# Performance work log

Hardware: AMD Instinct MI355X
Metric: run time of the kernel (lower is better)

Reference implementation:

```python
import jax, jax.numpy as jnp
import numpy as np

N = 50000        # num nodes
E = 800000       # num edges (before self-loops)
IN = 256         # in_channels
HID = 32         # hidden_channels per head
HEADS = 8
OUT = 64         # out_channels (layer 2, heads=1)
NEG_SLOPE = 0.2  # PyG GATConv default leaky_relu slope


def setup_inputs() -> dict:
    key = jax.random.key(0)
    ks = jax.random.split(key, 12)
    def rn(k, shape, scale=0.1):
        return jax.random.normal(k, shape, dtype=jnp.float32) * scale
    x = jax.random.normal(ks[0], (N, IN), dtype=jnp.float32)
    edge_index = jax.random.randint(ks[1], (2, E), 0, N, dtype=jnp.int64)
    return {
        "x": x,
        "edge_index": edge_index,
        # GATConv 1: in=256 -> 32 per head, 8 heads, concat
        "W1": rn(ks[2], (IN, HEADS * HID)),
        "att_src1": rn(ks[3], (HEADS, HID)),
        "att_dst1": rn(ks[4], (HEADS, HID)),
        "b1": jnp.zeros((HEADS * HID,), jnp.float32),
        # GATConv 2: in=256 -> 64, 1 head
        "W2": rn(ks[5], (HEADS * HID, OUT)),
        "att_src2": rn(ks[6], (1, OUT)),
        "att_dst2": rn(ks[7], (1, OUT)),
        "b2": jnp.zeros((OUT,), jnp.float32),
    }


def _gat_conv(x, src, dst, W, att_src, att_dst, bias, heads, out_ch):
    """PyG-style GATConv (add_self_loops already applied to src/dst).
    x: [N, F_in]; src/dst: [E']; returns [N, heads*out_ch] (concat)."""
    n = x.shape[0]
    h = (x @ W).reshape(n, heads, out_ch)                     # [N,H,F]
    a_src = jnp.einsum('nhf,hf->nh', h, att_src)              # [N,H]
    a_dst = jnp.einsum('nhf,hf->nh', h, att_dst)
    e = jax.nn.leaky_relu(a_src[src] + a_dst[dst], NEG_SLOPE)  # [E',H]
    # scatter-softmax over incoming edges of each dst node
    m = jax.ops.segment_max(e, dst, num_segments=n)            # [N,H]
    ex = jnp.exp(e - m[dst])
    denom = jax.ops.segment_sum(ex, dst, num_segments=n)       # [N,H]
    alpha = ex / denom[dst]                                    # [E',H]
    msg = alpha[:, :, None] * h[src]                           # [E',H,F]
    out = jax.ops.segment_sum(msg, dst, num_segments=n)        # [N,H,F]
    return out.reshape(n, heads * out_ch) + bias


def reference(x, edge_index, W1, att_src1, att_dst1, b1, W2, att_src2, att_dst2, b2):
    n = x.shape[0]
    loop = jnp.arange(n, dtype=edge_index.dtype)
    src = jnp.concatenate([edge_index[0], loop])  # add self-loops (PyG default)
    dst = jnp.concatenate([edge_index[1], loop])
    h = _gat_conv(x, src, dst, W1, att_src1, att_dst1, b1, HEADS, HID)
    h = jax.nn.relu(h)
    out = _gat_conv(h, src, dst, W2, att_src2, att_dst2, b2, 1, OUT)
    return out
```

## Files before the change

### kernel.cpp

```cpp
#include <hip/hip_runtime.h>
#include <hip/hip_bf16.h>


#define HEADS 8
#define HID 32
#define F1 256
#define F2 64
#define NEG_SLOPE 0.2f
#define SCAN_CHUNK 1024

typedef __attribute__((ext_vector_type(8))) short bf16x8;
typedef __attribute__((ext_vector_type(4))) float f32x4;
typedef __attribute__((ext_vector_type(8))) unsigned short u16x8;

__device__ __forceinline__ unsigned short f2b(float f) {
    union { float f; unsigned int i; } x; x.f = f;
    unsigned int r = x.i + 0x7fffu + ((x.i >> 16) & 1u);
    return (unsigned short)(r >> 16);
}
__device__ __forceinline__ float b2f(unsigned short u) {
    union { unsigned int i; float f; } x; x.i = ((unsigned int)u) << 16;
    return x.f;
}
__device__ __forceinline__ float leaky(float v) {
    return v > 0.f ? v : NEG_SLOPE * v;
}

__global__ void setup_kernel(const float* __restrict__ W1,
                             const float* __restrict__ W2,
                             unsigned short* __restrict__ W1T,
                             unsigned short* __restrict__ W2T,
                             int* __restrict__ deg, int Nn) {
    const int i = blockIdx.x * 256 + threadIdx.x;
    if (i < F1 * F1) {
        const int k = i >> 8, n = i & (F1 - 1);
        W1T[(size_t)n * F1 + k] = f2b(W1[i]);
    } else if (i < F1 * F1 + F1 * F2) {
        const int j = i - F1 * F1;
        const int k = j >> 6, n = j & (F2 - 1);
        W2T[(size_t)n * F1 + k] = f2b(W2[j]);
    } else if (i < F1 * F1 + F1 * F2 + Nn) {
        deg[i - F1 * F1 - F1 * F2] = 0;
    }
}

template<int BN, bool A_FP32, bool OUT_BF16>
__global__ __launch_bounds__(256) void mfma_gemm(
        const void* __restrict__ A,
        const unsigned short* __restrict__ BT,
        void* __restrict__ C, int M, int N, int K) {
    constexpr int BM = 128, BK = 32;
    __shared__ unsigned short As[BM * BK];
    __shared__ unsigned short Bs[BN * BK];
    const int tid = threadIdx.x;
    const int wave = tid >> 6, lane = tid & 63;
    const int quad = lane >> 4, l16 = lane & 15;
    const int brow = blockIdx.x * BM;
    const int bcol = blockIdx.y * BN;

    constexpr int MI = (BN == 128) ? 4 : 2;
    constexpr int NJ = 4;
    const int wm = (BN == 128) ? (wave & 1) * 64 : wave * 32;
    const int wn = (BN == 128) ? (wave >> 1) * 64 : 0;

    f32x4 acc[MI][NJ] = {};

    for (int k0 = 0; k0 < K; k0 += BK) {
#pragma unroll
        for (int it = 0; it < (BM * BK) / (256 * 8); ++it) {
            const int idx = it * 256 + tid;
            const int r = idx >> 2;
            const int kk = (idx & 3) * 8;
            const int gr = brow + r;
            if (A_FP32) {
                const float* Af = (const float*)A;
                float4 a0 = make_float4(0.f, 0.f, 0.f, 0.f);
                float4 a1 = make_float4(0.f, 0.f, 0.f, 0.f);
                if (gr < M) {
                    a0 = *(const float4*)&Af[(size_t)gr * K + k0 + kk];
                    a1 = *(const float4*)&Af[(size_t)gr * K + k0 + kk + 4];
                }
                ushort4 lo, hi;
                lo.x = f2b(a0.x); lo.y = f2b(a0.y); lo.z = f2b(a0.z); lo.w = f2b(a0.w);
                hi.x = f2b(a1.x); hi.y = f2b(a1.y); hi.z = f2b(a1.z); hi.w = f2b(a1.w);
                *(ushort4*)&As[r * BK + kk] = lo;
                *(ushort4*)&As[r * BK + kk + 4] = hi;
            } else {
                const unsigned short* Ab = (const unsigned short*)A;
                uint4 v = make_uint4(0u, 0u, 0u, 0u);
                if (gr < M) v = *(const uint4*)&Ab[(size_t)gr * K + k0 + kk];
                *(uint4*)&As[r * BK + kk] = v;
            }
        }
#pragma unroll
        for (int it = 0; it < (BN * BK) / (256 * 8); ++it) {
            const int idx = it * 256 + tid;
            const int r = idx >> 2;
            const int kk = (idx & 3) * 8;
            const uint4 v = *(const uint4*)&BT[(size_t)(bcol + r) * K + k0 + kk];
            *(uint4*)&Bs[r * BK + kk] = v;
        }
        __syncthreads();
        bf16x8 af[MI], bfr[NJ];
#pragma unroll
        for (int i = 0; i < MI; ++i)
            af[i] = *(const bf16x8*)&As[(wm + i * 16 + l16) * BK + quad * 8];
#pragma unroll
        for (int j = 0; j < NJ; ++j)
            bfr[j] = *(const bf16x8*)&Bs[(wn + j * 16 + l16) * BK + quad * 8];
#pragma unroll
        for (int i = 0; i < MI; ++i)
#pragma unroll
            for (int j = 0; j < NJ; ++j)
                acc[i][j] = __builtin_amdgcn_mfma_f32_16x16x32_bf16(
                    af[i], bfr[j], acc[i][j], 0, 0, 0);
        __syncthreads();
    }
#pragma unroll
    for (int i = 0; i < MI; ++i) {
#pragma unroll
        for (int r = 0; r < 4; ++r) {
            const int row = brow + wm + i * 16 + quad * 4 + r;
            if (row >= M) continue;
#pragma unroll
            for (int j = 0; j < NJ; ++j) {
                const int col = bcol + wn + j * 16 + l16;
                const float v = acc[i][j][r];
                if (OUT_BF16)
                    ((unsigned short*)C)[(size_t)row * N + col] = f2b(v);
                else
                    ((float*)C)[(size_t)row * N + col] = v;
            }
        }
    }
}

__global__ void att1_kernel(const unsigned short* __restrict__ h1b,
                            const float* __restrict__ att_src,
                            const float* __restrict__ att_dst,
                            float* __restrict__ a_src,
                            float* __restrict__ a_dst, int Nn) {
    const int i = blockIdx.x * blockDim.x + threadIdx.x;
    if (i >= Nn * HEADS) return;
    const int n = i >> 3, h = i & 7;
    const unsigned short* hp = h1b + (size_t)n * F1 + h * HID;
    const float* as = att_src + h * HID;
    const float* ad = att_dst + h * HID;
    float s = 0.f, d = 0.f;
#pragma unroll
    for (int f = 0; f < HID; ++f) {
        const float v = b2f(hp[f]);
        s += v * as[f];
        d += v * ad[f];
    }
    a_src[i] = s;
    a_dst[i] = d;
}

__global__ void att2_kernel(const unsigned short* __restrict__ h2b,
                            const float* __restrict__ att_src,
                            const float* __restrict__ att_dst,
                            float* __restrict__ a_src,
                            float* __restrict__ a_dst, int Nn) {
    const int n = blockIdx.x * blockDim.x + threadIdx.x;
    if (n >= Nn) return;
    const unsigned short* hp = h2b + (size_t)n * F2;
    float s = 0.f, d = 0.f;
#pragma unroll
    for (int f = 0; f < F2; ++f) {
        const float v = b2f(hp[f]);
        s += v * att_src[f];
        d += v * att_dst[f];
    }
    a_src[n] = s;
    a_dst[n] = d;
}

__global__ void hist_kernel(const int* __restrict__ ei, int E,
                            int* __restrict__ deg) {
    const int e = blockIdx.x * blockDim.x + threadIdx.x;
    if (e < E) atomicAdd(&deg[ei[E + e]], 1);
}

__global__ __launch_bounds__(256) void scan_bsum(const int* __restrict__ deg,
                                                 int* __restrict__ bsum, int Nn) {
    const int base = blockIdx.x * SCAN_CHUNK + threadIdx.x * 4;
    int s = 0;
#pragma unroll
    for (int j = 0; j < 4; ++j) {
        const int i = base + j;
        if (i < Nn) s += deg[i];
    }
#pragma unroll
    for (int off = 32; off > 0; off >>= 1) s += __shfl_down(s, off, 64);
    __shared__ int ws[4];
    if ((threadIdx.x & 63) == 0) ws[threadIdx.x >> 6] = s;
    __syncthreads();
    if (threadIdx.x == 0) bsum[blockIdx.x] = ws[0] + ws[1] + ws[2] + ws[3];
}

__global__ __launch_bounds__(256) void scan_boff(const int* __restrict__ bsum,
                                                 int* __restrict__ boff,
                                                 int* __restrict__ rowptr,
                                                 int B, int Nn) {
    __shared__ int sums[256];
    const int tid = threadIdx.x;
    const int v = (tid < B) ? bsum[tid] : 0;
    sums[tid] = v;
    __syncthreads();
    for (int off = 1; off < 256; off <<= 1) {
        const int cur = sums[tid];
        const int add = (tid >= off) ? sums[tid - off] : 0;
        __syncthreads();
        sums[tid] = cur + add;
        __syncthreads();
    }
    if (tid < B) boff[tid] = sums[tid] - v;
    if (tid == 255) rowptr[Nn] = sums[255];
}

__global__ __launch_bounds__(256) void scan_write(const int* __restrict__ deg,
                                                  const int* __restrict__ boff,
                                                  int* __restrict__ rowptr,
                                                  int* __restrict__ cursor, int Nn) {
    const int tid = threadIdx.x;
    const int base = blockIdx.x * SCAN_CHUNK + tid * 4;
    int v[4];
    int s = 0;
#pragma unroll
    for (int j = 0; j < 4; ++j) {
        const int i = base + j;
        v[j] = (i < Nn) ? deg[i] : 0;
        s += v[j];
    }
    __shared__ int sums[256];
    sums[tid] = s;
    __syncthreads();
    for (int off = 1; off < 256; off <<= 1) {
        const int cur = sums[tid];
        const int add = (tid >= off) ? sums[tid - off] : 0;
        __syncthreads();
        sums[tid] = cur + add;
        __syncthreads();
    }
    int off = boff[blockIdx.x] + sums[tid] - s;
#pragma unroll
    for (int j = 0; j < 4; ++j) {
        const int i = base + j;
        if (i < Nn) {
            rowptr[i] = off;
            cursor[i] = off;
            off += v[j];
        }
    }
}

__global__ void scatter_kernel(const int* __restrict__ ei, int E,
                               int* __restrict__ cursor,
                               int* __restrict__ csr_src) {
    const int e = blockIdx.x * blockDim.x + threadIdx.x;
    if (e >= E) return;
    const int d = ei[E + e];
    const int pos = atomicAdd(&cursor[d], 1);
    csr_src[pos] = ei[e];
}

__global__ __launch_bounds__(256) void gather1_kernel(
        const int* __restrict__ rowptr, const int* __restrict__ csr_src,
        const float* __restrict__ a_src, const float* __restrict__ a_dst,
        const unsigned short* __restrict__ h1b, const float* __restrict__ b1,
        unsigned short* __restrict__ out1b, int Nn) {
    const int lane = threadIdx.x & 63;
    const int sub  = lane >> 5;
    const int l    = lane & 31;
    int d = blockIdx.x * 8 + (threadIdx.x >> 6) * 2 + sub;
    const bool valid = d < Nn;
    if (!valid) d = Nn - 1;
    const int h = l >> 2;
    const int c = l * 8;

    const float adst = a_dst[d * HEADS + h];
    float acc[8];
    float denom;
    {
        const float w = __expf(leaky(a_src[d * HEADS + h] + adst));
        const u16x8 v = *(const u16x8*)&h1b[(size_t)d * F1 + c];
        denom = w;
#pragma unroll
        for (int q = 0; q < 8; ++q) acc[q] = w * b2f(v[q]);
    }
    const int beg = rowptr[d], end = rowptr[d + 1];
    int i = beg;
    for (; i + 4 <= end; i += 4) {
        int s[4];
        float e[4];
        u16x8 vv[4];
#pragma unroll
        for (int j = 0; j < 4; ++j) s[j] = csr_src[i + j];
#pragma unroll
        for (int j = 0; j < 4; ++j) e[j] = a_src[s[j] * HEADS + h];
#pragma unroll
        for (int j = 0; j < 4; ++j)
            vv[j] = *(const u16x8*)&h1b[(size_t)s[j] * F1 + c];
#pragma unroll
        for (int j = 0; j < 4; ++j) {
            const float w = __expf(leaky(e[j] + adst));
            denom += w;
#pragma unroll
            for (int q = 0; q < 8; ++q) acc[q] += w * b2f(vv[j][q]);
        }
    }
    for (; i < end; ++i) {
        const int s = csr_src[i];
        const float w = __expf(leaky(a_src[s * HEADS + h] + adst));
        const u16x8 v = *(const u16x8*)&h1b[(size_t)s * F1 + c];
        denom += w;
#pragma unroll
        for (int q = 0; q < 8; ++q) acc[q] += w * b2f(v[q]);
    }
    if (valid) {
        const float inv = 1.f / denom;
        u16x8 o;
#pragma unroll
        for (int q = 0; q < 8; ++q)
            o[q] = f2b(fmaxf(acc[q] * inv + b1[c + q], 0.f));
        *(u16x8*)&out1b[(size_t)d * F1 + c] = o;
    }
}

__global__ __launch_bounds__(256) void gather2_kernel(
        const int* __restrict__ rowptr, const int* __restrict__ csr_src,
        const float* __restrict__ a_src, const float* __restrict__ a_dst,
        const unsigned short* __restrict__ h2b, const float* __restrict__ b2,
        float* __restrict__ out, int Nn) {
    const int lane = threadIdx.x & 63;
    const int sub  = lane >> 4;
    const int l    = lane & 15;
    int d = blockIdx.x * 16 + (threadIdx.x >> 6) * 4 + sub;
    const bool valid = d < Nn;
    if (!valid) d = Nn - 1;
    const int c = l * 4;

    const float adst = a_dst[d];
    float a0, a1, a2, a3, denom;
    {
        const float w = __expf(leaky(a_src[d] + adst));
        const ushort4 v = *(const ushort4*)&h2b[(size_t)d * F2 + c];
        denom = w;
        a0 = w * b2f(v.x); a1 = w * b2f(v.y);
        a2 = w * b2f(v.z); a3 = w * b2f(v.w);
    }
    const int beg = rowptr[d], end = rowptr[d + 1];
    int i = beg;
    for (; i + 4 <= end; i += 4) {
        int s[4];
        float e[4];
        ushort4 vv[4];
#pragma unroll
        for (int j = 0; j < 4; ++j) s[j] = csr_src[i + j];
#pragma unroll
        for (int j = 0; j < 4; ++j) e[j] = a_src[s[j]];
#pragma unroll
        for (int j = 0; j < 4; ++j)
            vv[j] = *(const ushort4*)&h2b[(size_t)s[j] * F2 + c];
#pragma unroll
        for (int j = 0; j < 4; ++j) {
            const float w = __expf(leaky(e[j] + adst));
            denom += w;
            a0 += w * b2f(vv[j].x); a1 += w * b2f(vv[j].y);
            a2 += w * b2f(vv[j].z); a3 += w * b2f(vv[j].w);
        }
    }
    for (; i < end; ++i) {
        const int s = csr_src[i];
        const float w = __expf(leaky(a_src[s] + adst));
        const ushort4 v = *(const ushort4*)&h2b[(size_t)s * F2 + c];
        denom += w;
        a0 += w * b2f(v.x); a1 += w * b2f(v.y);
        a2 += w * b2f(v.z); a3 += w * b2f(v.w);
    }
    if (valid) {
        const float inv = 1.f / denom;
        float4 o;
        o.x = a0 * inv + b2[c + 0];
        o.y = a1 * inv + b2[c + 1];
        o.z = a2 * inv + b2[c + 2];
        o.w = a3 * inv + b2[c + 3];
        *(float4*)&out[(size_t)d * F2 + c] = o;
    }
}

extern "C" void kernel_launch(void* const* d_in, const int* in_sizes, int n_in,
                              void* d_out, int out_size, void* d_ws, size_t ws_size,
                              hipStream_t stream) {
    const float* x        = (const float*)d_in[0];
    const int*   ei       = (const int*)d_in[1];
    const float* W1       = (const float*)d_in[2];
    const float* att_src1 = (const float*)d_in[3];
    const float* att_dst1 = (const float*)d_in[4];
    const float* b1       = (const float*)d_in[5];
    const float* W2       = (const float*)d_in[6];
    const float* att_src2 = (const float*)d_in[7];
    const float* att_dst2 = (const float*)d_in[8];
    const float* b2       = (const float*)d_in[9];
    float* out = (float*)d_out;

    const int Nn = in_sizes[0] / F1;
    const int E  = in_sizes[1] / 2;
    const int NB = (Nn + SCAN_CHUNK - 1) / SCAN_CHUNK;

    char* p = (char*)d_ws;
    unsigned short* h1b   = (unsigned short*)p; p += (size_t)Nn * F1 * 2;
    unsigned short* out1b = (unsigned short*)p; p += (size_t)Nn * F1 * 2;
    unsigned short* W1T   = (unsigned short*)p; p += (size_t)F1 * F1 * 2;
    unsigned short* W2T   = (unsigned short*)p; p += (size_t)F2 * F1 * 2;
    unsigned short* h2b   = (unsigned short*)p; p += (size_t)Nn * F2 * 2;
    float* a_src1 = (float*)p; p += (size_t)Nn * HEADS * 4;
    float* a_dst1 = (float*)p; p += (size_t)Nn * HEADS * 4;
    float* a_src2 = (float*)p; p += (size_t)Nn * 4;
    float* a_dst2 = (float*)p; p += (size_t)Nn * 4;
    int* deg     = (int*)p; p += (size_t)Nn * 4;
    int* rowptr  = (int*)p; p += (size_t)(Nn + 1) * 4;
    int* cursor  = (int*)p; p += (size_t)Nn * 4;
    int* bsum    = (int*)p; p += 256 * 4;
    int* boff    = (int*)p; p += 256 * 4;
    int* csr_src = (int*)p; p += (size_t)E * 4;

    {
        const int total = F1 * F1 + F1 * F2 + Nn;
        setup_kernel<<<(total + 255) / 256, 256, 0, stream>>>(
            W1, W2, W1T, W2T, deg, Nn);
    }

    hist_kernel<<<(E + 255) / 256, 256, 0, stream>>>(ei, E, deg);
    scan_bsum<<<NB, 256, 0, stream>>>(deg, bsum, Nn);
    scan_boff<<<1, 256, 0, stream>>>(bsum, boff, rowptr, NB, Nn);
    scan_write<<<NB, 256, 0, stream>>>(deg, boff, rowptr, cursor, Nn);
    scatter_kernel<<<(E + 255) / 256, 256, 0, stream>>>(ei, E, cursor, csr_src);

    {
        dim3 grid((Nn + 127) / 128, F1 / 128);
        mfma_gemm<128, true, true><<<grid, 256, 0, stream>>>(
            x, W1T, h1b, Nn, F1, F1);
    }
    att1_kernel<<<(Nn * HEADS + 255) / 256, 256, 0, stream>>>(
        h1b, att_src1, att_dst1, a_src1, a_dst1, Nn);
    gather1_kernel<<<(Nn + 7) / 8, 256, 0, stream>>>(
        rowptr, csr_src, a_src1, a_dst1, h1b, b1, out1b, Nn);

    {
        dim3 grid((Nn + 127) / 128, F2 / 64);
        mfma_gemm<64, false, true><<<grid, 256, 0, stream>>>(
            out1b, W2T, h2b, Nn, F2, F1);
    }
    att2_kernel<<<(Nn + 255) / 256, 256, 0, stream>>>(
        h2b, att_src2, att_dst2, a_src2, a_dst2, Nn);
    gather2_kernel<<<(Nn + 15) / 16, 256, 0, stream>>>(
        rowptr, csr_src, a_src2, a_dst2, h2b, b2, out, Nn);
}
```

Baseline: 336.2 us.

## Store layer-1 features head-major and gather per head with edge-parallel lanes

```diff
diff --git a/kernel.cpp b/kernel.cpp
--- a/kernel.cpp
+++ b/kernel.cpp
@@ -44,7 +44,7 @@
     }
 }
 
-template<int BN, bool A_FP32, bool OUT_BF16>
+template<int BN, bool A_FP32, int OUT_MODE>
 __global__ __launch_bounds__(256) void mfma_gemm(
         const void* __restrict__ A,
         const unsigned short* __restrict__ BT,
@@ -126,24 +126,28 @@
             for (int j = 0; j < NJ; ++j) {
                 const int col = bcol + wn + j * 16 + l16;
                 const float v = acc[i][j][r];
-                if (OUT_BF16)
+                if (OUT_MODE == 0) {
+                    ((float*)C)[(size_t)row * N + col] = v;
+                } else if (OUT_MODE == 1) {
                     ((unsigned short*)C)[(size_t)row * N + col] = f2b(v);
-                else
-                    ((float*)C)[(size_t)row * N + col] = v;
+                } else {
+                    ((unsigned short*)C)[((size_t)(col >> 5) * M + row) * HID
+                                         + (col & 31)] = f2b(v);
+                }
             }
         }
     }
 }
 
-__global__ void att1_kernel(const unsigned short* __restrict__ h1b,
+__global__ void att1_kernel(const unsigned short* __restrict__ h1hm,
                             const float* __restrict__ att_src,
                             const float* __restrict__ att_dst,
                             float* __restrict__ a_src,
                             float* __restrict__ a_dst, int Nn) {
-    const int i = blockIdx.x * blockDim.x + threadIdx.x;
-    if (i >= Nn * HEADS) return;
-    const int n = i >> 3, h = i & 7;
-    const unsigned short* hp = h1b + (size_t)n * F1 + h * HID;
+    const int n = blockIdx.x * blockDim.x + threadIdx.x;
+    const int h = blockIdx.y;
+    if (n >= Nn) return;
+    const unsigned short* hp = h1hm + ((size_t)h * Nn + n) * HID;
     const float* as = att_src + h * HID;
     const float* ad = att_dst + h * HID;
     float s = 0.f, d = 0.f;
@@ -153,8 +157,8 @@
         s += v * as[f];
         d += v * ad[f];
     }
-    a_src[i] = s;
-    a_dst[i] = d;
+    a_src[(size_t)h * Nn + n] = s;
+    a_dst[(size_t)h * Nn + n] = d;
 }
 
 __global__ void att2_kernel(const unsigned short* __restrict__ h2b,
@@ -268,63 +272,54 @@
 __global__ __launch_bounds__(256) void gather1_kernel(
         const int* __restrict__ rowptr, const int* __restrict__ csr_src,
         const float* __restrict__ a_src, const float* __restrict__ a_dst,
-        const unsigned short* __restrict__ h1b, const float* __restrict__ b1,
+        const unsigned short* __restrict__ h1hm, const float* __restrict__ b1,
         unsigned short* __restrict__ out1b, int Nn) {
+    const int h = blockIdx.x & 7;
+    const int d = (blockIdx.x >> 3) * 4 + (threadIdx.x >> 6);
+    if (d >= Nn) return;
     const int lane = threadIdx.x & 63;
-    const int sub  = lane >> 5;
-    const int l    = lane & 31;
-    int d = blockIdx.x * 8 + (threadIdx.x >> 6) * 2 + sub;
-    const bool valid = d < Nn;
-    if (!valid) d = Nn - 1;
-    const int h = l >> 2;
-    const int c = l * 8;
-
-    const float adst = a_dst[d * HEADS + h];
-    float acc[8];
-    float denom;
-    {
-        const float w = __expf(leaky(a_src[d * HEADS + h] + adst));
-        const u16x8 v = *(const u16x8*)&h1b[(size_t)d * F1 + c];
-        denom = w;
-#pragma unroll
-        for (int q = 0; q < 8; ++q) acc[q] = w * b2f(v[q]);
-    }
+    const int j  = lane >> 3;
+    const int cl = lane & 7;
+
+    const unsigned short* hh = h1hm + (size_t)h * Nn * HID;
+    const float* asrc = a_src + (size_t)h * Nn;
+    const float adst = a_dst[(size_t)h * Nn + d];
+
     const int beg = rowptr[d], end = rowptr[d + 1];
-    int i = beg;
-    for (; i + 4 <= end; i += 4) {
-        int s[4];
-        float e[4];
-        u16x8 vv[4];
-#pragma unroll
-        for (int j = 0; j < 4; ++j) s[j] = csr_src[i + j];
-#pragma unroll
-        for (int j = 0; j < 4; ++j) e[j] = a_src[s[j] * HEADS + h];
-#pragma unroll
-        for (int j = 0; j < 4; ++j)
-            vv[j] = *(const u16x8*)&h1b[(size_t)s[j] * F1 + c];
-#pragma unroll
-        for (int j = 0; j < 4; ++j) {
-            const float w = __expf(leaky(e[j] + adst));
-            denom += w;
-#pragma unroll
-            for (int q = 0; q < 8; ++q) acc[q] += w * b2f(vv[j][q]);
-        }
-    }
-    for (; i < end; ++i) {
-        const int s = csr_src[i];
-        const float w = __expf(leaky(a_src[s * HEADS + h] + adst));
-        const u16x8 v = *(const u16x8*)&h1b[(size_t)s * F1 + c];
-        denom += w;
-#pragma unroll
-        for (int q = 0; q < 8; ++q) acc[q] += w * b2f(v[q]);
-    }
-    if (valid) {
-        const float inv = 1.f / denom;
-        u16x8 o;
-#pragma unroll
-        for (int q = 0; q < 8; ++q)
-            o[q] = f2b(fmaxf(acc[q] * inv + b1[c + q], 0.f));
-        *(u16x8*)&out1b[(size_t)d * F1 + c] = o;
+    float a0 = 0.f, a1 = 0.f, a2 = 0.f, a3 = 0.f, wsum = 0.f;
+    for (int i = beg; i < end; i += 8) {
+        const int idx = i + j;
+        const bool ok = idx < end;
+        const int s = ok ? __builtin_nontemporal_load(&csr_src[idx]) : d;
+        const float e = asrc[s];
+        const ushort4 v = *(const ushort4*)&hh[(size_t)s * HID + cl * 4];
+        float w = __expf(leaky(e + adst));
+        w = ok ? w : 0.f;
+        wsum += w;
+        a0 += w * b2f(v.x); a1 += w * b2f(v.y);
+        a2 += w * b2f(v.z); a3 += w * b2f(v.w);
+    }
+#pragma unroll
+    for (int off = 8; off < 64; off <<= 1) {
+        a0 += __shfl_xor(a0, off, 64);
+        a1 += __shfl_xor(a1, off, 64);
+        a2 += __shfl_xor(a2, off, 64);
+        a3 += __shfl_xor(a3, off, 64);
+        wsum += __shfl_xor(wsum, off, 64);
+    }
+    const float ws = __expf(leaky(asrc[d] + adst));
+    const ushort4 sv = *(const ushort4*)&hh[(size_t)d * HID + cl * 4];
+    a0 += ws * b2f(sv.x); a1 += ws * b2f(sv.y);
+    a2 += ws * b2f(sv.z); a3 += ws * b2f(sv.w);
+    const float inv = 1.f / (wsum + ws);
+    if (j == 0) {
+        const int c = h * HID + cl * 4;
+        ushort4 o;
+        o.x = f2b(fmaxf(a0 * inv + b1[c + 0], 0.f));
+        o.y = f2b(fmaxf(a1 * inv + b1[c + 1], 0.f));
+        o.z = f2b(fmaxf(a2 * inv + b1[c + 2], 0.f));
+        o.w = f2b(fmaxf(a3 * inv + b1[c + 3], 0.f));
+        *(ushort4*)&out1b[(size_t)d * F1 + c] = o;
     }
 }
 
@@ -357,18 +352,18 @@
         float e[4];
         ushort4 vv[4];
 #pragma unroll
-        for (int j = 0; j < 4; ++j) s[j] = csr_src[i + j];
-#pragma unroll
-        for (int j = 0; j < 4; ++j) e[j] = a_src[s[j]];
-#pragma unroll
-        for (int j = 0; j < 4; ++j)
-            vv[j] = *(const ushort4*)&h2b[(size_t)s[j] * F2 + c];
-#pragma unroll
-        for (int j = 0; j < 4; ++j) {
-            const float w = __expf(leaky(e[j] + adst));
+        for (int jj = 0; jj < 4; ++jj) s[jj] = csr_src[i + jj];
+#pragma unroll
+        for (int jj = 0; jj < 4; ++jj) e[jj] = a_src[s[jj]];
+#pragma unroll
+        for (int jj = 0; jj < 4; ++jj)
+            vv[jj] = *(const ushort4*)&h2b[(size_t)s[jj] * F2 + c];
+#pragma unroll
+        for (int jj = 0; jj < 4; ++jj) {
+            const float w = __expf(leaky(e[jj] + adst));
             denom += w;
-            a0 += w * b2f(vv[j].x); a1 += w * b2f(vv[j].y);
-            a2 += w * b2f(vv[j].z); a3 += w * b2f(vv[j].w);
+            a0 += w * b2f(vv[jj].x); a1 += w * b2f(vv[jj].y);
+            a2 += w * b2f(vv[jj].z); a3 += w * b2f(vv[jj].w);
         }
     }
     for (; i < end; ++i) {
@@ -410,7 +405,7 @@
     const int NB = (Nn + SCAN_CHUNK - 1) / SCAN_CHUNK;
 
     char* p = (char*)d_ws;
-    unsigned short* h1b   = (unsigned short*)p; p += (size_t)Nn * F1 * 2;
+    unsigned short* h1hm  = (unsigned short*)p; p += (size_t)Nn * F1 * 2;
     unsigned short* out1b = (unsigned short*)p; p += (size_t)Nn * F1 * 2;
     unsigned short* W1T   = (unsigned short*)p; p += (size_t)F1 * F1 * 2;
     unsigned short* W2T   = (unsigned short*)p; p += (size_t)F2 * F1 * 2;
@@ -440,17 +435,20 @@
 
     {
         dim3 grid((Nn + 127) / 128, F1 / 128);
-        mfma_gemm<128, true, true><<<grid, 256, 0, stream>>>(
-            x, W1T, h1b, Nn, F1, F1);
-    }
-    att1_kernel<<<(Nn * HEADS + 255) / 256, 256, 0, stream>>>(
-        h1b, att_src1, att_dst1, a_src1, a_dst1, Nn);
-    gather1_kernel<<<(Nn + 7) / 8, 256, 0, stream>>>(
-        rowptr, csr_src, a_src1, a_dst1, h1b, b1, out1b, Nn);
+        mfma_gemm<128, true, 2><<<grid, 256, 0, stream>>>(
+            x, W1T, h1hm, Nn, F1, F1);
+    }
+    {
+        dim3 grid((Nn + 255) / 256, HEADS);
+        att1_kernel<<<grid, 256, 0, stream>>>(
+            h1hm, att_src1, att_dst1, a_src1, a_dst1, Nn);
+    }
+    gather1_kernel<<<((Nn + 3) / 4) * 8, 256, 0, stream>>>(
+        rowptr, csr_src, a_src1, a_dst1, h1hm, b1, out1b, Nn);
 
     {
         dim3 grid((Nn + 127) / 128, F2 / 64);
-        mfma_gemm<64, false, true><<<grid, 256, 0, stream>>>(
+        mfma_gemm<64, false, 1><<<grid, 256, 0, stream>>>(
             out1b, W2T, h2b, Nn, F2, F1);
     }
     att2_kernel<<<(Nn + 255) / 256, 256, 0, stream>>>(
```

Measured after the change: 440.0 us. 1.31x slower.
